# Kernel tuning notes

Measured on AMD Instinct MI355X. Metric: run time of the kernel, lower is better.

## Reference

```python
import jax, jax.numpy as jnp
import numpy as np
from jax import lax

B, N, D, H, E, K, FF = 4, 1024, 1024, 16, 12, 2, 4
HD = D // H
EPS_LN = 1e-5


def setup_inputs() -> dict:
    key = jax.random.key(0)
    ks = jax.random.split(key, 10)
    s = 0.02
    return {
        "x": jax.random.normal(ks[0], (B, N, D), jnp.float32),
        "Wr": jax.random.normal(ks[1], (E, D), jnp.float32) * s,          # router [E, D] (no bias)
        "Wq": jax.random.normal(ks[2], (E, D, D), jnp.float32) * s,       # per-expert [out, in]
        "Wk": jax.random.normal(ks[3], (E, D, D), jnp.float32) * s,
        "Wv": jax.random.normal(ks[4], (E, D, D), jnp.float32) * s,
        "Wo": jax.random.normal(ks[5], (E, D, D), jnp.float32) * s,
        "W1": jax.random.normal(ks[6], (FF * D, D), jnp.float32) * s,
        "b1": jnp.zeros((FF * D,), jnp.float32),
        "W2": jax.random.normal(ks[7], (D, FF * D), jnp.float32) * s,
        "b2": jnp.zeros((D,), jnp.float32),
        "g1": jnp.ones((D,), jnp.float32),
        "be1": jnp.zeros((D,), jnp.float32),
        "g2": jnp.ones((D,), jnp.float32),
        "be2": jnp.zeros((D,), jnp.float32),
    }


def _ln(x, g, b):
    m = jnp.mean(x, axis=-1, keepdims=True)
    v = jnp.mean(jnp.square(x - m), axis=-1, keepdims=True)
    return (x - m) * lax.rsqrt(v + EPS_LN) * g + b


def _moe_mix(inp, W, combine):
    """sum_e combine[:, e] * (inp @ W[e].T) via scan over the E experts.
    inp: [T, Din], W: [E, Dout, Din], combine: [T, E] -> [T, Dout]"""
    def body(acc, ec):
        We, ce = ec
        return acc + ce[:, None] * (inp @ We.T), None
    acc0 = jnp.zeros((inp.shape[0], W.shape[1]), inp.dtype)
    acc, _ = lax.scan(body, acc0, (W, jnp.swapaxes(combine, 0, 1)))
    return acc


def _moe_attention(x, Wr, Wq, Wk, Wv, Wo):
    x_flat = x.reshape(-1, D)                     # [T, D]
    T = x_flat.shape[0]
    logits = x_flat @ Wr.T                        # [T, E]
    probs = jax.nn.softmax(logits, axis=-1)
    topv, topi = lax.top_k(probs, K)              # [T, K]
    topv = topv / (jnp.sum(topv, axis=-1, keepdims=True) + 1e-6)
    # dense combine weights [T, E] (zero for unselected experts)
    combine = jnp.zeros((T, E), x.dtype).at[jnp.arange(T)[:, None], topi].add(topv)

    q = _moe_mix(x_flat, Wq, combine)
    k = _moe_mix(x_flat, Wk, combine)
    v = _moe_mix(x_flat, Wv, combine)

    # [B, H, N, HD]
    q = q.reshape(B, N, H, HD).transpose(0, 2, 1, 3)
    k = k.reshape(B, N, H, HD).transpose(0, 2, 1, 3)
    v = v.reshape(B, N, H, HD).transpose(0, 2, 1, 3)
    scores = jnp.einsum("bhqd,bhkd->bhqk", q, k) / jnp.sqrt(jnp.asarray(HD, x.dtype))
    attn = jax.nn.softmax(scores, axis=-1)
    out = jnp.einsum("bhqk,bhkd->bhqd", attn, v)
    out_flat = out.transpose(0, 2, 1, 3).reshape(T, D)

    o = _moe_mix(out_flat, Wo, combine)           # expert output projection

    # load-balance loss (no grad in original: computed under torch.no_grad)
    counts = jnp.zeros((E,), x.dtype).at[topi.ravel()].add(1.0)
    p = probs.sum(axis=0)
    lb = jax.lax.stop_gradient((counts / (counts.sum() + 1e-6) * p).sum() * E)
    return o.reshape(B, N, D), lb


def reference(x, Wr, Wq, Wk, Wv, Wo, W1, b1, W2, b2, g1, be1, g2, be2):
    # pre-norm transformer block: x + MoEAttn(LN(x)); + FFN(LN(.))
    attn_out, lb = _moe_attention(_ln(x, g1, be1), Wr, Wq, Wk, Wv, Wo)
    h = x + attn_out
    hn = _ln(h, g2, be2)
    ff = (jax.nn.gelu(hn @ W1.T + b1)) @ W2.T + b2   # dropout=0 (eval)
    y = h + ff
    return y, lb
```

## Files before the change

kernel.cpp:

```cpp
#include <hip/hip_runtime.h>

#define B_ 4
#define N_ 1024
#define D_ 1024
#define H_ 16
#define HD_ 64
#define E_ 12
#define T_ 4096
#define FF_ 4096

static constexpr size_t SZ_ = (size_t)T_ * D_;

typedef __attribute__((ext_vector_type(8))) short bhalf8;
typedef __attribute__((ext_vector_type(4))) float f32x4;

#define GLDS(gp, lp)                                                         \
  __builtin_amdgcn_global_load_lds(                                          \
      (const __attribute__((address_space(1))) void*)(gp),                   \
      (__attribute__((address_space(3))) void*)(lp), 16, 0, 0)

__device__ __forceinline__ float wave_sum64(float v) {
#pragma unroll
  for (int o = 32; o > 0; o >>= 1) v += __shfl_down(v, o);
  return v;
}

__device__ __forceinline__ unsigned short f2bf(float f) {
  unsigned u = __float_as_uint(f);
  u += 0x7FFFu + ((u >> 16) & 1u);
  return (unsigned short)(u >> 16);
}
__device__ __forceinline__ float b2f(unsigned short s) {
  return __uint_as_float(((unsigned)s) << 16);
}
__device__ __forceinline__ unsigned addpair_bf(unsigned x, unsigned y) {
  float lo = b2f((unsigned short)(x & 0xffff)) + b2f((unsigned short)(y & 0xffff));
  float hi = b2f((unsigned short)(x >> 16)) + b2f((unsigned short)(y >> 16));
  return (unsigned)f2bf(lo) | ((unsigned)f2bf(hi) << 16);
}

__device__ __forceinline__ float gelu_f(float x) {
  float u = 0.7978845608028654f * (x + 0.044715f * x * x * x);
  u = fminf(fmaxf(u, -15.f), 15.f);
  float e = __expf(2.f * u);
  float th = (e - 1.f) / (e + 1.f);
  return 0.5f * x * (1.f + th);
}

__device__ __forceinline__ int slot_of(int row, int q) {
  return row * 4 + (q ^ ((row >> 1) & 3));
}

__global__ __launch_bounds__(256) void ln_kernel(const float* __restrict__ x,
    const float* __restrict__ g, const float* __restrict__ b,
    float* __restrict__ out, unsigned short* __restrict__ outb) {
  const int t = blockIdx.x, tid = threadIdx.x;
  const size_t base = (size_t)t * D_;
  const float4 v = ((const float4*)(x + base))[tid];
  float s = v.x + v.y + v.z + v.w;
  float s2 = v.x * v.x + v.y * v.y + v.z * v.z + v.w * v.w;
  s = wave_sum64(s);
  s2 = wave_sum64(s2);
  __shared__ float ls[4], ls2[4];
  const int w = tid >> 6;
  if ((tid & 63) == 0) { ls[w] = s; ls2[w] = s2; }
  __syncthreads();
  const float mean = (ls[0] + ls[1] + ls[2] + ls[3]) * (1.0f / D_);
  const float var = (ls2[0] + ls2[1] + ls2[2] + ls2[3]) * (1.0f / D_) - mean * mean;
  const float inv = rsqrtf(var + 1e-5f);
  const float4 gg = ((const float4*)g)[tid];
  const float4 bb = ((const float4*)b)[tid];
  float4 o4;
  o4.x = (v.x - mean) * inv * gg.x + bb.x;
  o4.y = (v.y - mean) * inv * gg.y + bb.y;
  o4.z = (v.z - mean) * inv * gg.z + bb.z;
  o4.w = (v.w - mean) * inv * gg.w + bb.w;
  ((float4*)(out + base))[tid] = o4;
  ushort4 u4;
  u4.x = f2bf(o4.x); u4.y = f2bf(o4.y); u4.z = f2bf(o4.z); u4.w = f2bf(o4.w);
  ((ushort4*)(outb + base))[tid] = u4;
}

__global__ __launch_bounds__(256) void hln2_kernel(const float* __restrict__ x,
    const unsigned short* __restrict__ oa, const unsigned short* __restrict__ ob,
    const float* __restrict__ g, const float* __restrict__ be,
    float* __restrict__ hout, unsigned short* __restrict__ hnb) {
  const int t = blockIdx.x, tid = threadIdx.x;
  const size_t base = (size_t)t * D_;
  const float4 xv = ((const float4*)(x + base))[tid];
  const ushort4 av = ((const ushort4*)(oa + base))[tid];
  const ushort4 bv = ((const ushort4*)(ob + base))[tid];
  float4 hv;
  hv.x = xv.x + b2f(av.x) + b2f(bv.x);
  hv.y = xv.y + b2f(av.y) + b2f(bv.y);
  hv.z = xv.z + b2f(av.z) + b2f(bv.z);
  hv.w = xv.w + b2f(av.w) + b2f(bv.w);
  ((float4*)(hout + base))[tid] = hv;
  float s = hv.x + hv.y + hv.z + hv.w;
  float s2 = hv.x * hv.x + hv.y * hv.y + hv.z * hv.z + hv.w * hv.w;
  s = wave_sum64(s);
  s2 = wave_sum64(s2);
  __shared__ float ls[4], ls2[4];
  const int w = tid >> 6;
  if ((tid & 63) == 0) { ls[w] = s; ls2[w] = s2; }
  __syncthreads();
  const float mean = (ls[0] + ls[1] + ls[2] + ls[3]) * (1.0f / D_);
  const float var = (ls2[0] + ls2[1] + ls2[2] + ls2[3]) * (1.0f / D_) - mean * mean;
  const float inv = rsqrtf(var + 1e-5f);
  const float4 gg = ((const float4*)g)[tid];
  const float4 bb = ((const float4*)be)[tid];
  ushort4 o4;
  o4.x = f2bf((hv.x - mean) * inv * gg.x + bb.x);
  o4.y = f2bf((hv.y - mean) * inv * gg.y + bb.y);
  o4.z = f2bf((hv.z - mean) * inv * gg.z + bb.z);
  o4.w = f2bf((hv.w - mean) * inv * gg.w + bb.w);
  ((ushort4*)(hnb + base))[tid] = o4;
}

__global__ __launch_bounds__(256) void router_logits(const float* __restrict__ xn,
    const float* __restrict__ Wr, float* __restrict__ probs,
    int* __restrict__ topi, float2* __restrict__ topw) {
  const int t = blockIdx.x, tid = threadIdx.x;
  const float4 xv = ((const float4*)(xn + (size_t)t * D_))[tid];
  float acc[E_];
#pragma unroll
  for (int e = 0; e < E_; ++e) {
    const float4 wv = ((const float4*)(Wr + (size_t)e * D_))[tid];
    acc[e] = xv.x * wv.x + xv.y * wv.y + xv.z * wv.z + xv.w * wv.w;
  }
#pragma unroll
  for (int e = 0; e < E_; ++e) acc[e] = wave_sum64(acc[e]);
  __shared__ float red[4][E_];
  const int w = tid >> 6;
  if ((tid & 63) == 0) {
#pragma unroll
    for (int e = 0; e < E_; ++e) red[w][e] = acc[e];
  }
  __syncthreads();
  if (tid == 0) {
    float lg[E_];
    float mx = -1e30f;
#pragma unroll
    for (int e = 0; e < E_; ++e) {
      lg[e] = red[0][e] + red[1][e] + red[2][e] + red[3][e];
      mx = fmaxf(mx, lg[e]);
    }
    float p[E_];
    float sum = 0.f;
#pragma unroll
    for (int e = 0; e < E_; ++e) { p[e] = __expf(lg[e] - mx); sum += p[e]; }
    const float invs = 1.f / sum;
#pragma unroll
    for (int e = 0; e < E_; ++e) {
      p[e] *= invs;
      probs[t * E_ + e] = p[e];
    }
    int i0 = 0;
#pragma unroll
    for (int e = 1; e < E_; ++e) if (p[e] > p[i0]) i0 = e;
    int i1 = (i0 == 0) ? 1 : 0;
#pragma unroll
    for (int e = 0; e < E_; ++e) if (e != i0 && p[e] > p[i1]) i1 = e;
    const float rs = 1.f / (p[i0] + p[i1] + 1e-6f);
    topi[t] = i0 | (i1 << 8);
    topw[t] = make_float2(p[i0] * rs, p[i1] * rs);
  }
}

__global__ __launch_bounds__(256) void psum_kernel(const float* __restrict__ probs,
                                                   float* __restrict__ psum) {
  const int tid = threadIdx.x;
  float local[E_] = {};
  for (int t = tid; t < T_; t += 256) {
#pragma unroll
    for (int e = 0; e < E_; ++e) local[e] += probs[t * E_ + e];
  }
#pragma unroll
  for (int e = 0; e < E_; ++e) local[e] = wave_sum64(local[e]);
  __shared__ float red[4][E_];
  const int w = tid >> 6;
  if ((tid & 63) == 0) {
#pragma unroll
    for (int e = 0; e < E_; ++e) red[w][e] = local[e];
  }
  __syncthreads();
  if (tid < E_)
    psum[tid] = red[0][tid] + red[1][tid] + red[2][tid] + red[3][tid];
}

__global__ __launch_bounds__(256) void build_lists(const int* __restrict__ topi,
    const float2* __restrict__ topw, int* __restrict__ ecnt,
    int* __restrict__ etok, float* __restrict__ ewt) {
  const int e = blockIdx.x;
  const int tid = threadIdx.x;
  const int wid = tid >> 6, lane = tid & 63;
  __shared__ int wbase[4];
  __shared__ int base;
  if (tid == 0) base = 0;
  __syncthreads();
  for (int c = 0; c < T_; c += 256) {
    const int t = c + tid;
    const int pk = topi[t];
    const int i0 = pk & 0xFF, i1 = (pk >> 8) & 0xFF;
    const float2 w2 = topw[t];
    const int sel = (i0 == e) ? 0 : ((i1 == e) ? 1 : -1);
    const unsigned long long mask = __ballot(sel >= 0);
    const int prefix = __popcll(mask & ((1ULL << lane) - 1ULL));
    if (lane == 0) wbase[wid] = __popcll(mask);
    __syncthreads();
    if (tid == 0) {
      int s = base;
#pragma unroll
      for (int ww = 0; ww < 4; ++ww) { int cc = wbase[ww]; wbase[ww] = s; s += cc; }
      base = s;
    }
    __syncthreads();
    if (sel >= 0) {
      const int pos = wbase[wid] + prefix;
      etok[e * T_ + pos] = t | (sel << 16);
      ewt[e * T_ + pos] = sel ? w2.y : w2.x;
    }
    __syncthreads();
  }
  if (tid == 0) ecnt[e] = base;
}

__global__ __launch_bounds__(256) void cvtw_kernel(const float* __restrict__ src,
    unsigned short* __restrict__ dst) {
  const size_t i = (size_t)blockIdx.x * 256 + threadIdx.x;
  const float4 v = ((const float4*)src)[i];
  ushort4 o;
  o.x = f2bf(v.x); o.y = f2bf(v.y); o.z = f2bf(v.z); o.w = f2bf(v.w);
  ((ushort4*)dst)[i] = o;
}

__global__ __launch_bounds__(256) void moe_mfma(const unsigned short* __restrict__ Ab,
    const float* __restrict__ Wall, unsigned short* __restrict__ out,
    size_t kkStride, const int* __restrict__ ecnt, const int* __restrict__ etok,
    const float* __restrict__ ewt) {
  const int e = blockIdx.z;
  const int Me = ecnt[e];
  const int m0 = blockIdx.y * 128;
  if (m0 >= Me) return;
  const int n0 = blockIdx.x * 128;
  const float* W = Wall + (size_t)e * D_ * D_;
  __shared__ __align__(16) unsigned short As[128 * 32];
  __shared__ __align__(16) unsigned short Bs[128 * 32];
  __shared__ int stok[128];
  __shared__ float swt[128];
  const int tid = threadIdx.x;
  if (tid < 128) {
    const int s = m0 + tid;
    if (s < Me) { stok[tid] = etok[e * T_ + s]; swt[tid] = ewt[e * T_ + s]; }
    else        { stok[tid] = 0;                swt[tid] = 0.f; }
  }
  __syncthreads();
  const int s0 = tid, s1 = tid + 256;
  const int r0 = s0 >> 2, q0 = (s0 & 3) ^ ((r0 >> 1) & 3);
  const int r1 = s1 >> 2, q1 = (s1 & 3) ^ ((r1 >> 1) & 3);
  const unsigned short* aP0 = Ab + (size_t)(stok[r0] & 0xFFFF) * D_ + q0 * 8;
  const unsigned short* aP1 = Ab + (size_t)(stok[r1] & 0xFFFF) * D_ + q1 * 8;
  const float* bP0 = W + (size_t)(n0 + r0) * D_ + q0 * 8;
  const float* bP1 = W + (size_t)(n0 + r1) * D_ + q1 * 8;
  char* AsC = (char*)As;
  char* BsC = (char*)Bs;
  const int wave = tid >> 6, lane = tid & 63;
  const int wm0 = (wave >> 1) * 64, wn0 = (wave & 1) * 64;
  const int lr = lane & 15, lq = lane >> 4;
  int aoff[4], boff[4];
#pragma unroll
  for (int t = 0; t < 4; ++t) {
    aoff[t] = slot_of(wm0 + t * 16 + lr, lq) * 16;
    boff[t] = slot_of(wn0 + t * 16 + lr, lq) * 16;
  }
  f32x4 acc[4][4];
#pragma unroll
  for (int i = 0; i < 4; ++i)
#pragma unroll
    for (int j = 0; j < 4; ++j) acc[i][j] = (f32x4){0.f, 0.f, 0.f, 0.f};
  for (int kt = 0; kt < D_; kt += 32) {
    __syncthreads();
    GLDS(aP0 + kt, AsC + s0 * 16);
    GLDS(aP1 + kt, AsC + s1 * 16);
    const float4 f0 = *(const float4*)(bP0 + kt);
    const float4 f1 = *(const float4*)(bP0 + kt + 4);
    const float4 f2 = *(const float4*)(bP1 + kt);
    const float4 f3 = *(const float4*)(bP1 + kt + 4);
    bhalf8 w0, w1;
    w0[0] = (short)f2bf(f0.x); w0[1] = (short)f2bf(f0.y);
    w0[2] = (short)f2bf(f0.z); w0[3] = (short)f2bf(f0.w);
    w0[4] = (short)f2bf(f1.x); w0[5] = (short)f2bf(f1.y);
    w0[6] = (short)f2bf(f1.z); w0[7] = (short)f2bf(f1.w);
    w1[0] = (short)f2bf(f2.x); w1[1] = (short)f2bf(f2.y);
    w1[2] = (short)f2bf(f2.z); w1[3] = (short)f2bf(f2.w);
    w1[4] = (short)f2bf(f3.x); w1[5] = (short)f2bf(f3.y);
    w1[6] = (short)f2bf(f3.z); w1[7] = (short)f2bf(f3.w);
    *(bhalf8*)(BsC + s0 * 16) = w0;
    *(bhalf8*)(BsC + s1 * 16) = w1;
    __syncthreads();
    bhalf8 af[4], bfr[4];
#pragma unroll
    for (int t = 0; t < 4; ++t) af[t] = *(const bhalf8*)(AsC + aoff[t]);
#pragma unroll
    for (int t = 0; t < 4; ++t) bfr[t] = *(const bhalf8*)(BsC + boff[t]);
#pragma unroll
    for (int i = 0; i < 4; ++i)
#pragma unroll
      for (int j = 0; j < 4; ++j)
        acc[i][j] = __builtin_amdgcn_mfma_f32_16x16x32_bf16(af[i], bfr[j], acc[i][j], 0, 0, 0);
  }
#pragma unroll
  for (int mt = 0; mt < 4; ++mt)
#pragma unroll
    for (int nt = 0; nt < 4; ++nt) {
      const f32x4 c = acc[mt][nt];
      const int col = n0 + wn0 + nt * 16 + lr;
#pragma unroll
      for (int r = 0; r < 4; ++r) {
        const int row = wm0 + mt * 16 + lq * 4 + r;
        if (m0 + row < Me) {
          const int pk = stok[row];
          out[(size_t)(pk >> 16) * kkStride + (size_t)(pk & 0xFFFF) * D_ + col] =
              f2bf(c[r] * swt[row]);
        }
      }
    }
}

__global__ __launch_bounds__(256) void ffn1_mfma(const unsigned short* __restrict__ Ab,
    const unsigned short* __restrict__ Bb, const float* __restrict__ bias,
    unsigned short* __restrict__ mid) {
  const int m0 = blockIdx.y * 128, n0 = blockIdx.x * 128;
  __shared__ __align__(16) unsigned short As[128 * 32];
  __shared__ __align__(16) unsigned short Bs[128 * 32];
  const int tid = threadIdx.x;
  const int s0 = tid, s1 = tid + 256;
  const int r0 = s0 >> 2, q0 = (s0 & 3) ^ ((r0 >> 1) & 3);
  const int r1 = s1 >> 2, q1 = (s1 & 3) ^ ((r1 >> 1) & 3);
  const unsigned short* aP0 = Ab + (size_t)(m0 + r0) * D_ + q0 * 8;
  const unsigned short* aP1 = Ab + (size_t)(m0 + r1) * D_ + q1 * 8;
  const unsigned short* bP0 = Bb + (size_t)(n0 + r0) * D_ + q0 * 8;
  const unsigned short* bP1 = Bb + (size_t)(n0 + r1) * D_ + q1 * 8;
  char* AsC = (char*)As;
  char* BsC = (char*)Bs;
  const int wave = tid >> 6, lane = tid & 63;
  const int wm0 = (wave >> 1) * 64, wn0 = (wave & 1) * 64;
  const int lr = lane & 15, lq = lane >> 4;
  int aoff[4], boff[4];
#pragma unroll
  for (int t = 0; t < 4; ++t) {
    aoff[t] = slot_of(wm0 + t * 16 + lr, lq) * 16;
    boff[t] = slot_of(wn0 + t * 16 + lr, lq) * 16;
  }
  f32x4 acc[4][4];
#pragma unroll
  for (int i = 0; i < 4; ++i)
#pragma unroll
    for (int j = 0; j < 4; ++j) acc[i][j] = (f32x4){0.f, 0.f, 0.f, 0.f};
  for (int kt = 0; kt < D_; kt += 32) {
    __syncthreads();
    GLDS(aP0 + kt, AsC + s0 * 16);
    GLDS(aP1 + kt, AsC + s1 * 16);
    GLDS(bP0 + kt, BsC + s0 * 16);
    GLDS(bP1 + kt, BsC + s1 * 16);
    __syncthreads();
    bhalf8 af[4], bfr[4];
#pragma unroll
    for (int t = 0; t < 4; ++t) af[t] = *(const bhalf8*)(AsC + aoff[t]);
#pragma unroll
    for (int t = 0; t < 4; ++t) bfr[t] = *(const bhalf8*)(BsC + boff[t]);
#pragma unroll
    for (int i = 0; i < 4; ++i)
#pragma unroll
      for (int j = 0; j < 4; ++j)
        acc[i][j] = __builtin_amdgcn_mfma_f32_16x16x32_bf16(af[i], bfr[j], acc[i][j], 0, 0, 0);
  }
  float bcol[4];
#pragma unroll
  for (int nt = 0; nt < 4; ++nt) bcol[nt] = bias[n0 + wn0 + nt * 16 + lr];
#pragma unroll
  for (int mt = 0; mt < 4; ++mt)
#pragma unroll
    for (int nt = 0; nt < 4; ++nt) {
      const f32x4 c = acc[mt][nt];
      const int col = n0 + wn0 + nt * 16 + lr;
#pragma unroll
      for (int r = 0; r < 4; ++r) {
        const int row = m0 + wm0 + mt * 16 + lq * 4 + r;
        mid[(size_t)row * FF_ + col] = f2bf(gelu_f(c[r] + bcol[nt]));
      }
    }
}

__global__ __launch_bounds__(256) void ffn2_mfma(const unsigned short* __restrict__ Ab,
    const unsigned short* __restrict__ Bb, const float* __restrict__ bias,
    const float* __restrict__ hres, float* __restrict__ y) {
  const int m0 = blockIdx.y * 128, n0 = blockIdx.x * 128;
  __shared__ __align__(16) unsigned short As[128 * 32];
  __shared__ __align__(16) unsigned short Bs[128 * 32];
  const int tid = threadIdx.x;
  const int s0 = tid, s1 = tid + 256;
  const int r0 = s0 >> 2, q0 = (s0 & 3) ^ ((r0 >> 1) & 3);
  const int r1 = s1 >> 2, q1 = (s1 & 3) ^ ((r1 >> 1) & 3);
  const unsigned short* aP0 = Ab + (size_t)(m0 + r0) * FF_ + q0 * 8;
  const unsigned short* aP1 = Ab + (size_t)(m0 + r1) * FF_ + q1 * 8;
  const unsigned short* bP0 = Bb + (size_t)(n0 + r0) * FF_ + q0 * 8;
  const unsigned short* bP1 = Bb + (size_t)(n0 + r1) * FF_ + q1 * 8;
  char* AsC = (char*)As;
  char* BsC = (char*)Bs;
  const int wave = tid >> 6, lane = tid & 63;
  const int wm0 = (wave >> 1) * 64, wn0 = (wave & 1) * 64;
  const int lr = lane & 15, lq = lane >> 4;
  int aoff[4], boff[4];
#pragma unroll
  for (int t = 0; t < 4; ++t) {
    aoff[t] = slot_of(wm0 + t * 16 + lr, lq) * 16;
    boff[t] = slot_of(wn0 + t * 16 + lr, lq) * 16;
  }
  f32x4 acc[4][4];
#pragma unroll
  for (int i = 0; i < 4; ++i)
#pragma unroll
    for (int j = 0; j < 4; ++j) acc[i][j] = (f32x4){0.f, 0.f, 0.f, 0.f};
  for (int kt = 0; kt < FF_; kt += 32) {
    __syncthreads();
    GLDS(aP0 + kt, AsC + s0 * 16);
    GLDS(aP1 + kt, AsC + s1 * 16);
    GLDS(bP0 + kt, BsC + s0 * 16);
    GLDS(bP1 + kt, BsC + s1 * 16);
    __syncthreads();
    bhalf8 af[4], bfr[4];
#pragma unroll
    for (int t = 0; t < 4; ++t) af[t] = *(const bhalf8*)(AsC + aoff[t]);
#pragma unroll
    for (int t = 0; t < 4; ++t) bfr[t] = *(const bhalf8*)(BsC + boff[t]);
#pragma unroll
    for (int i = 0; i < 4; ++i)
#pragma unroll
      for (int j = 0; j < 4; ++j)
        acc[i][j] = __builtin_amdgcn_mfma_f32_16x16x32_bf16(af[i], bfr[j], acc[i][j], 0, 0, 0);
  }
  float bcol[4];
#pragma unroll
  for (int nt = 0; nt < 4; ++nt) bcol[nt] = bias[n0 + wn0 + nt * 16 + lr];
#pragma unroll
  for (int mt = 0; mt < 4; ++mt)
#pragma unroll
    for (int nt = 0; nt < 4; ++nt) {
      const f32x4 c = acc[mt][nt];
      const int col = n0 + wn0 + nt * 16 + lr;
#pragma unroll
      for (int r = 0; r < 4; ++r) {
        const int row = m0 + wm0 + mt * 16 + lq * 4 + r;
        const size_t idx = (size_t)row * D_ + col;
        y[idx] = c[r] + bcol[nt] + hres[idx];
      }
    }
}

__global__ __launch_bounds__(256) void add2b_kernel(unsigned short* __restrict__ a,
    const unsigned short* __restrict__ b) {
  const size_t i = (size_t)blockIdx.x * 256 + threadIdx.x;
  uint4 av = ((uint4*)a)[i];
  const uint4 bv = ((const uint4*)b)[i];
  av.x = addpair_bf(av.x, bv.x);
  av.y = addpair_bf(av.y, bv.y);
  av.z = addpair_bf(av.z, bv.z);
  av.w = addpair_bf(av.w, bv.w);
  ((uint4*)a)[i] = av;
}

__global__ __launch_bounds__(256) void attn_kernel(const unsigned short* __restrict__ q,
    const unsigned short* __restrict__ k, const unsigned short* __restrict__ v,
    unsigned short* __restrict__ out) {
  const int bh = blockIdx.x;
  const int b = bh >> 4, h = bh & 15;
  const int q0 = blockIdx.y * 64;
  const int tid = threadIdx.x;
  const int wave = tid >> 6, lane = tid & 63;
  const int lc = lane & 15, lg = lane >> 4;

  __shared__ __align__(16) unsigned short Ks[64 * 64];
  __shared__ __align__(16) unsigned short Vt[64 * 64];
  __shared__ __align__(16) unsigned short Pl[4][16 * 64];
  char* const KsC = (char*)Ks;
  char* const VtC = (char*)Vt;
  char* const PlC = (char*)&Pl[wave][0];

  bhalf8 qf0, qf1;
  {
    const unsigned short* qp =
        q + ((size_t)(b * N_ + q0 + wave * 16 + lc)) * D_ + h * HD_ + lg * 8;
    qf0 = *(const bhalf8*)qp;
    qf1 = *(const bhalf8*)(qp + 32);
  }

  int off[4][2];
#pragma unroll
  for (int t = 0; t < 4; ++t)
#pragma unroll
    for (int ch = 0; ch < 2; ++ch)
      off[t][ch] = (t * 16 + lc) * 128 + (((ch * 4 + lg) ^ (lc & 7)) << 4);

  const int krow = tid >> 2, ks0 = tid & 3;
  const unsigned short* const kgp =
      k + ((size_t)(b * N_ + krow)) * D_ + h * HD_ + ks0 * 8;
  const int kwo0 = krow * 128 + ((ks0 ^ (krow & 7)) << 4);
  const int kwo1 = krow * 128 + (((ks0 ^ 4) ^ (krow & 7)) << 4);
  const int vkv = (tid & 31) * 2, vd0 = (tid >> 5) * 8;
  const unsigned short* const vgp =
      v + ((size_t)(b * N_ + vkv)) * D_ + h * HD_ + vd0;
  int vwo[8];
#pragma unroll
  for (int c = 0; c < 8; ++c) {
    const int d = vd0 + c;
    vwo[c] = d * 128 + ((((vkv >> 3) ^ (d & 7)) << 4)) + (vkv & 7) * 2;
  }

  float m_i[4], l_i[4];
  f32x4 o_acc[4];
#pragma unroll
  for (int r = 0; r < 4; ++r) { m_i[r] = -3.0e38f; l_i[r] = 0.f; }
#pragma unroll
  for (int t = 0; t < 4; ++t) o_acc[t] = (f32x4){0.f, 0.f, 0.f, 0.f};

  uint4 ka = *(const uint4*)(kgp);
  uint4 kb = *(const uint4*)(kgp + 32);
  uint4 va = *(const uint4*)(vgp);
  uint4 vb = *(const uint4*)(vgp + D_);

  for (int kt = 0; kt < 16; ++kt) {
    __syncthreads();
    *(uint4*)(KsC + kwo0) = ka;
    *(uint4*)(KsC + kwo1) = kb;
    {
      const unsigned av4[4] = {va.x, va.y, va.z, va.w};
      const unsigned bv4[4] = {vb.x, vb.y, vb.z, vb.w};
#pragma unroll
      for (int c = 0; c < 4; ++c) {
        const unsigned w0 = (av4[c] & 0xffffu) | (bv4[c] << 16);
        const unsigned w1 = (av4[c] >> 16) | (bv4[c] & 0xffff0000u);
        *(unsigned*)(VtC + vwo[2 * c]) = w0;
        *(unsigned*)(VtC + vwo[2 * c + 1]) = w1;
      }
    }
    __syncthreads();
    if (kt < 15) {
      const size_t go = (size_t)(kt + 1) * 64 * D_;
      ka = *(const uint4*)(kgp + go);
      kb = *(const uint4*)(kgp + go + 32);
      va = *(const uint4*)(vgp + go);
      vb = *(const uint4*)(vgp + go + D_);
    }
    f32x4 s4[4];
#pragma unroll
    for (int t = 0; t < 4; ++t) {
      f32x4 acc = (f32x4){0.f, 0.f, 0.f, 0.f};
      acc = __builtin_amdgcn_mfma_f32_16x16x32_bf16(
          qf0, *(const bhalf8*)(KsC + off[t][0]), acc, 0, 0, 0);
      acc = __builtin_amdgcn_mfma_f32_16x16x32_bf16(
          qf1, *(const bhalf8*)(KsC + off[t][1]), acc, 0, 0, 0);
      s4[t] = acc;
    }
    float alpha[4];
#pragma unroll
    for (int r = 0; r < 4; ++r) {
      const float e0 = s4[0][r] * 0.125f, e1 = s4[1][r] * 0.125f;
      const float e2 = s4[2][r] * 0.125f, e3 = s4[3][r] * 0.125f;
      float mt = fmaxf(fmaxf(e0, e1), fmaxf(e2, e3));
#pragma unroll
      for (int o = 8; o > 0; o >>= 1) mt = fmaxf(mt, __shfl_xor(mt, o));
      const float mn = fmaxf(m_i[r], mt);
      alpha[r] = __expf(m_i[r] - mn);
      m_i[r] = mn;
      const float p0 = __expf(e0 - mn), p1 = __expf(e1 - mn);
      const float p2 = __expf(e2 - mn), p3 = __expf(e3 - mn);
      float rs = p0 + p1 + p2 + p3;
#pragma unroll
      for (int o = 8; o > 0; o >>= 1) rs += __shfl_xor(rs, o);
      l_i[r] = l_i[r] * alpha[r] + rs;
      const int qrow = 4 * lg + r;
      const int rb = qrow * 128 + (lc & 7) * 2;
      const int sw = qrow & 7;
      *(unsigned short*)(PlC + rb + (((0 + (lc >> 3)) ^ sw) << 4)) = f2bf(p0);
      *(unsigned short*)(PlC + rb + (((2 + (lc >> 3)) ^ sw) << 4)) = f2bf(p1);
      *(unsigned short*)(PlC + rb + (((4 + (lc >> 3)) ^ sw) << 4)) = f2bf(p2);
      *(unsigned short*)(PlC + rb + (((6 + (lc >> 3)) ^ sw) << 4)) = f2bf(p3);
    }
#pragma unroll
    for (int t = 0; t < 4; ++t) {
      f32x4 o = o_acc[t];
      o[0] *= alpha[0]; o[1] *= alpha[1]; o[2] *= alpha[2]; o[3] *= alpha[3];
      o_acc[t] = o;
    }
    const bhalf8 pf0 = *(const bhalf8*)(PlC + off[0][0]);
    const bhalf8 pf1 = *(const bhalf8*)(PlC + off[0][1]);
#pragma unroll
    for (int t = 0; t < 4; ++t) {
      o_acc[t] = __builtin_amdgcn_mfma_f32_16x16x32_bf16(
          pf0, *(const bhalf8*)(VtC + off[t][0]), o_acc[t], 0, 0, 0);
      o_acc[t] = __builtin_amdgcn_mfma_f32_16x16x32_bf16(
          pf1, *(const bhalf8*)(VtC + off[t][1]), o_acc[t], 0, 0, 0);
    }
  }
  const size_t obase = ((size_t)(b * N_ + q0 + wave * 16)) * D_ + h * HD_;
#pragma unroll
  for (int r = 0; r < 4; ++r) {
    const float inv = 1.f / l_i[r];
    const size_t rbase = obase + (size_t)(4 * lg + r) * D_;
#pragma unroll
    for (int t = 0; t < 4; ++t)
      out[rbase + t * 16 + lc] = f2bf(o_acc[t][r] * inv);
  }
}

__global__ void lb_kernel(const int* __restrict__ ecnt,
                          const float* __restrict__ psum, float* __restrict__ out) {
  if (threadIdx.x == 0 && blockIdx.x == 0) {
    float tot = 0.f;
    for (int e = 0; e < E_; ++e) tot += (float)ecnt[e];
    float s = 0.f;
    for (int e = 0; e < E_; ++e) s += (float)ecnt[e] / (tot + 1e-6f) * psum[e];
    out[0] = s * (float)E_;
  }
}

extern "C" void kernel_launch(void* const* d_in, const int* in_sizes, int n_in,
                              void* d_out, int out_size, void* d_ws, size_t ws_size,
                              hipStream_t stream) {
  (void)in_sizes; (void)n_in; (void)out_size; (void)ws_size;
  const float* x  = (const float*)d_in[0];
  const float* Wr = (const float*)d_in[1];
  const float* Wq = (const float*)d_in[2];
  const float* Wk = (const float*)d_in[3];
  const float* Wv = (const float*)d_in[4];
  const float* Wo = (const float*)d_in[5];
  const float* W1 = (const float*)d_in[6];
  const float* b1 = (const float*)d_in[7];
  const float* W2 = (const float*)d_in[8];
  const float* b2 = (const float*)d_in[9];
  const float* g1 = (const float*)d_in[10];
  const float* be1 = (const float*)d_in[11];
  const float* g2 = (const float*)d_in[12];
  const float* be2 = (const float*)d_in[13];
  float* y = (float*)d_out;

  char* p = (char*)d_ws;
  float* xn = (float*)p;                 p += SZ_ * 4;
  unsigned short* xnb = (unsigned short*)p;  p += SZ_ * 2;
  unsigned short* q2b = (unsigned short*)p;  p += 2 * SZ_ * 2;
  unsigned short* k2b = (unsigned short*)p;  p += 2 * SZ_ * 2;
  unsigned short* v2b = (unsigned short*)p;  p += 2 * SZ_ * 2;
  unsigned short* attb = (unsigned short*)p; p += SZ_ * 2;
  unsigned short* W1b = (unsigned short*)p;  p += (size_t)FF_ * D_ * 2;
  unsigned short* W2b = (unsigned short*)p;  p += (size_t)FF_ * D_ * 2;
  float* psum = (float*)p;               p += E_ * 4;
  int* ecnt = (int*)p;                   p += E_ * 4;
  int* etok = (int*)p;                   p += (size_t)E_ * T_ * 4;
  float* ewt = (float*)p;                p += (size_t)E_ * T_ * 4;
  float* probs = (float*)p;              p += (size_t)T_ * E_ * 4;
  int* topi = (int*)p;                   p += T_ * 4;
  float2* topw = (float2*)p;
  unsigned short* o2b  = q2b;
  float* hbuf          = (float*)k2b;
  unsigned short* hnb  = v2b;
  unsigned short* midb = (unsigned short*)d_ws;

  ln_kernel<<<T_, 256, 0, stream>>>(x, g1, be1, xn, xnb);
  cvtw_kernel<<<(FF_ * D_) / 1024, 256, 0, stream>>>(W1, W1b);
  cvtw_kernel<<<(FF_ * D_) / 1024, 256, 0, stream>>>(W2, W2b);
  router_logits<<<T_, 256, 0, stream>>>(xn, Wr, probs, topi, topw);
  psum_kernel<<<1, 256, 0, stream>>>(probs, psum);
  build_lists<<<E_, 256, 0, stream>>>(topi, topw, ecnt, etok, ewt);
  dim3 gmoe(D_ / 128, T_ / 128, E_);
  moe_mfma<<<gmoe, 256, 0, stream>>>(xnb, Wq, q2b, SZ_, ecnt, etok, ewt);
  moe_mfma<<<gmoe, 256, 0, stream>>>(xnb, Wk, k2b, SZ_, ecnt, etok, ewt);
  moe_mfma<<<gmoe, 256, 0, stream>>>(xnb, Wv, v2b, SZ_, ecnt, etok, ewt);
  add2b_kernel<<<SZ_ / 2048, 256, 0, stream>>>(q2b, q2b + SZ_);
  add2b_kernel<<<SZ_ / 2048, 256, 0, stream>>>(k2b, k2b + SZ_);
  add2b_kernel<<<SZ_ / 2048, 256, 0, stream>>>(v2b, v2b + SZ_);
  attn_kernel<<<dim3(B_ * H_, N_ / 64), 256, 0, stream>>>(q2b, k2b, v2b, attb);
  moe_mfma<<<gmoe, 256, 0, stream>>>(attb, Wo, o2b, SZ_, ecnt, etok, ewt);
  hln2_kernel<<<T_, 256, 0, stream>>>(x, o2b, o2b + SZ_, g2, be2, hbuf, hnb);
  ffn1_mfma<<<dim3(FF_ / 128, T_ / 128), 256, 0, stream>>>(hnb, W1b, b1, midb);
  ffn2_mfma<<<dim3(D_ / 128, T_ / 128), 256, 0, stream>>>(midb, W2b, b2, hbuf, y);
  lb_kernel<<<1, 64, 0, stream>>>(ecnt, psum, y + SZ_);
}
```

Baseline: 734.5 us.

## Pre-convert expert weights to bf16, fuse LN into router, split-K FFN2

Each expert weight stack (Wq/Wk/Wv/Wo) is now converted to bf16 by its own pass into a shared buffer, so moe_mfma can load B tiles directly into LDS instead of converting fp32 inside the inner loop. The router now recomputes LayerNorm itself, which drops the fp32 normalized-activation buffer. The residual plus b2 is written to y early in hln2. FFN2 is split along K into two partial-sum kernels joined by an add3 pass, doubling the grid. The cost is four extra full weight-conversion passes and extra partial-buffer traffic.

Result: faster. 680.8 us (-7.3%).

```diff
diff --git a/kernel.cpp b/kernel.cpp
--- a/kernel.cpp
+++ b/kernel.cpp
@@ -53,7 +53,7 @@
 
 __global__ __launch_bounds__(256) void ln_kernel(const float* __restrict__ x,
     const float* __restrict__ g, const float* __restrict__ b,
-    float* __restrict__ out, unsigned short* __restrict__ outb) {
+    unsigned short* __restrict__ outb) {
   const int t = blockIdx.x, tid = threadIdx.x;
   const size_t base = (size_t)t * D_;
   const float4 v = ((const float4*)(x + base))[tid];
@@ -70,21 +70,19 @@
   const float inv = rsqrtf(var + 1e-5f);
   const float4 gg = ((const float4*)g)[tid];
   const float4 bb = ((const float4*)b)[tid];
-  float4 o4;
-  o4.x = (v.x - mean) * inv * gg.x + bb.x;
-  o4.y = (v.y - mean) * inv * gg.y + bb.y;
-  o4.z = (v.z - mean) * inv * gg.z + bb.z;
-  o4.w = (v.w - mean) * inv * gg.w + bb.w;
-  ((float4*)(out + base))[tid] = o4;
   ushort4 u4;
-  u4.x = f2bf(o4.x); u4.y = f2bf(o4.y); u4.z = f2bf(o4.z); u4.w = f2bf(o4.w);
+  u4.x = f2bf((v.x - mean) * inv * gg.x + bb.x);
+  u4.y = f2bf((v.y - mean) * inv * gg.y + bb.y);
+  u4.z = f2bf((v.z - mean) * inv * gg.z + bb.z);
+  u4.w = f2bf((v.w - mean) * inv * gg.w + bb.w);
   ((ushort4*)(outb + base))[tid] = u4;
 }
 
 __global__ __launch_bounds__(256) void hln2_kernel(const float* __restrict__ x,
     const unsigned short* __restrict__ oa, const unsigned short* __restrict__ ob,
     const float* __restrict__ g, const float* __restrict__ be,
-    float* __restrict__ hout, unsigned short* __restrict__ hnb) {
+    const float* __restrict__ b2, float* __restrict__ y,
+    unsigned short* __restrict__ hnb) {
   const int t = blockIdx.x, tid = threadIdx.x;
   const size_t base = (size_t)t * D_;
   const float4 xv = ((const float4*)(x + base))[tid];
@@ -95,7 +93,11 @@
   hv.y = xv.y + b2f(av.y) + b2f(bv.y);
   hv.z = xv.z + b2f(av.z) + b2f(bv.z);
   hv.w = xv.w + b2f(av.w) + b2f(bv.w);
-  ((float4*)(hout + base))[tid] = hv;
+  const float4 b2v = ((const float4*)b2)[tid];
+  float4 yv;
+  yv.x = hv.x + b2v.x; yv.y = hv.y + b2v.y;
+  yv.z = hv.z + b2v.z; yv.w = hv.w + b2v.w;
+  ((float4*)(y + base))[tid] = yv;
   float s = hv.x + hv.y + hv.z + hv.w;
   float s2 = hv.x * hv.x + hv.y * hv.y + hv.z * hv.z + hv.w * hv.w;
   s = wave_sum64(s);
@@ -117,21 +119,39 @@
   ((ushort4*)(hnb + base))[tid] = o4;
 }
 
-__global__ __launch_bounds__(256) void router_logits(const float* __restrict__ xn,
+__global__ __launch_bounds__(256) void router_ln(const float* __restrict__ x,
+    const float* __restrict__ g, const float* __restrict__ b,
     const float* __restrict__ Wr, float* __restrict__ probs,
     int* __restrict__ topi, float2* __restrict__ topw) {
   const int t = blockIdx.x, tid = threadIdx.x;
-  const float4 xv = ((const float4*)(xn + (size_t)t * D_))[tid];
+  const float4 xv = ((const float4*)(x + (size_t)t * D_))[tid];
+  float s = xv.x + xv.y + xv.z + xv.w;
+  float s2 = xv.x * xv.x + xv.y * xv.y + xv.z * xv.z + xv.w * xv.w;
+  s = wave_sum64(s);
+  s2 = wave_sum64(s2);
+  __shared__ float ls[4], ls2[4];
+  const int w = tid >> 6;
+  if ((tid & 63) == 0) { ls[w] = s; ls2[w] = s2; }
+  __syncthreads();
+  const float mean = (ls[0] + ls[1] + ls[2] + ls[3]) * (1.0f / D_);
+  const float var = (ls2[0] + ls2[1] + ls2[2] + ls2[3]) * (1.0f / D_) - mean * mean;
+  const float inv = rsqrtf(var + 1e-5f);
+  const float4 gg = ((const float4*)g)[tid];
+  const float4 bb = ((const float4*)b)[tid];
+  float4 xn4;
+  xn4.x = (xv.x - mean) * inv * gg.x + bb.x;
+  xn4.y = (xv.y - mean) * inv * gg.y + bb.y;
+  xn4.z = (xv.z - mean) * inv * gg.z + bb.z;
+  xn4.w = (xv.w - mean) * inv * gg.w + bb.w;
   float acc[E_];
 #pragma unroll
   for (int e = 0; e < E_; ++e) {
     const float4 wv = ((const float4*)(Wr + (size_t)e * D_))[tid];
-    acc[e] = xv.x * wv.x + xv.y * wv.y + xv.z * wv.z + xv.w * wv.w;
+    acc[e] = xn4.x * wv.x + xn4.y * wv.y + xn4.z * wv.z + xn4.w * wv.w;
   }
 #pragma unroll
   for (int e = 0; e < E_; ++e) acc[e] = wave_sum64(acc[e]);
   __shared__ float red[4][E_];
-  const int w = tid >> 6;
   if ((tid & 63) == 0) {
 #pragma unroll
     for (int e = 0; e < E_; ++e) red[w][e] = acc[e];
@@ -235,7 +255,7 @@
 }
 
 __global__ __launch_bounds__(256) void moe_mfma(const unsigned short* __restrict__ Ab,
-    const float* __restrict__ Wall, unsigned short* __restrict__ out,
+    const unsigned short* __restrict__ Wb, unsigned short* __restrict__ out,
     size_t kkStride, const int* __restrict__ ecnt, const int* __restrict__ etok,
     const float* __restrict__ ewt) {
   const int e = blockIdx.z;
@@ -243,7 +263,7 @@
   const int m0 = blockIdx.y * 128;
   if (m0 >= Me) return;
   const int n0 = blockIdx.x * 128;
-  const float* W = Wall + (size_t)e * D_ * D_;
+  const unsigned short* W = Wb + (size_t)e * D_ * D_;
   __shared__ __align__(16) unsigned short As[128 * 32];
   __shared__ __align__(16) unsigned short Bs[128 * 32];
   __shared__ int stok[128];
@@ -260,8 +280,8 @@
   const int r1 = s1 >> 2, q1 = (s1 & 3) ^ ((r1 >> 1) & 3);
   const unsigned short* aP0 = Ab + (size_t)(stok[r0] & 0xFFFF) * D_ + q0 * 8;
   const unsigned short* aP1 = Ab + (size_t)(stok[r1] & 0xFFFF) * D_ + q1 * 8;
-  const float* bP0 = W + (size_t)(n0 + r0) * D_ + q0 * 8;
-  const float* bP1 = W + (size_t)(n0 + r1) * D_ + q1 * 8;
+  const unsigned short* bP0 = W + (size_t)(n0 + r0) * D_ + q0 * 8;
+  const unsigned short* bP1 = W + (size_t)(n0 + r1) * D_ + q1 * 8;
   char* AsC = (char*)As;
   char* BsC = (char*)Bs;
   const int wave = tid >> 6, lane = tid & 63;
@@ -282,21 +302,8 @@
     __syncthreads();
     GLDS(aP0 + kt, AsC + s0 * 16);
     GLDS(aP1 + kt, AsC + s1 * 16);
-    const float4 f0 = *(const float4*)(bP0 + kt);
-    const float4 f1 = *(const float4*)(bP0 + kt + 4);
-    const float4 f2 = *(const float4*)(bP1 + kt);
-    const float4 f3 = *(const float4*)(bP1 + kt + 4);
-    bhalf8 w0, w1;
-    w0[0] = (short)f2bf(f0.x); w0[1] = (short)f2bf(f0.y);
-    w0[2] = (short)f2bf(f0.z); w0[3] = (short)f2bf(f0.w);
-    w0[4] = (short)f2bf(f1.x); w0[5] = (short)f2bf(f1.y);
-    w0[6] = (short)f2bf(f1.z); w0[7] = (short)f2bf(f1.w);
-    w1[0] = (short)f2bf(f2.x); w1[1] = (short)f2bf(f2.y);
-    w1[2] = (short)f2bf(f2.z); w1[3] = (short)f2bf(f2.w);
-    w1[4] = (short)f2bf(f3.x); w1[5] = (short)f2bf(f3.y);
-    w1[6] = (short)f2bf(f3.z); w1[7] = (short)f2bf(f3.w);
-    *(bhalf8*)(BsC + s0 * 16) = w0;
-    *(bhalf8*)(BsC + s1 * 16) = w1;
+    GLDS(bP0 + kt, BsC + s0 * 16);
+    GLDS(bP1 + kt, BsC + s1 * 16);
     __syncthreads();
     bhalf8 af[4], bfr[4];
 #pragma unroll
@@ -392,20 +399,22 @@
     }
 }
 
-__global__ __launch_bounds__(256) void ffn2_mfma(const unsigned short* __restrict__ Ab,
-    const unsigned short* __restrict__ Bb, const float* __restrict__ bias,
-    const float* __restrict__ hres, float* __restrict__ y) {
+__global__ __launch_bounds__(256) void ffn2_split(const unsigned short* __restrict__ Ab,
+    const unsigned short* __restrict__ Bb, float* __restrict__ part0,
+    float* __restrict__ part1) {
   const int m0 = blockIdx.y * 128, n0 = blockIdx.x * 128;
+  const int k0 = blockIdx.z * (FF_ / 2);
+  float* const part = blockIdx.z ? part1 : part0;
   __shared__ __align__(16) unsigned short As[128 * 32];
   __shared__ __align__(16) unsigned short Bs[128 * 32];
   const int tid = threadIdx.x;
   const int s0 = tid, s1 = tid + 256;
   const int r0 = s0 >> 2, q0 = (s0 & 3) ^ ((r0 >> 1) & 3);
   const int r1 = s1 >> 2, q1 = (s1 & 3) ^ ((r1 >> 1) & 3);
-  const unsigned short* aP0 = Ab + (size_t)(m0 + r0) * FF_ + q0 * 8;
-  const unsigned short* aP1 = Ab + (size_t)(m0 + r1) * FF_ + q1 * 8;
-  const unsigned short* bP0 = Bb + (size_t)(n0 + r0) * FF_ + q0 * 8;
-  const unsigned short* bP1 = Bb + (size_t)(n0 + r1) * FF_ + q1 * 8;
+  const unsigned short* aP0 = Ab + (size_t)(m0 + r0) * FF_ + q0 * 8 + k0;
+  const unsigned short* aP1 = Ab + (size_t)(m0 + r1) * FF_ + q1 * 8 + k0;
+  const unsigned short* bP0 = Bb + (size_t)(n0 + r0) * FF_ + q0 * 8 + k0;
+  const unsigned short* bP1 = Bb + (size_t)(n0 + r1) * FF_ + q1 * 8 + k0;
   char* AsC = (char*)As;
   char* BsC = (char*)Bs;
   const int wave = tid >> 6, lane = tid & 63;
@@ -422,7 +431,7 @@
   for (int i = 0; i < 4; ++i)
 #pragma unroll
     for (int j = 0; j < 4; ++j) acc[i][j] = (f32x4){0.f, 0.f, 0.f, 0.f};
-  for (int kt = 0; kt < FF_; kt += 32) {
+  for (int kt = 0; kt < FF_ / 2; kt += 32) {
     __syncthreads();
     GLDS(aP0 + kt, AsC + s0 * 16);
     GLDS(aP1 + kt, AsC + s1 * 16);
@@ -440,9 +449,6 @@
       for (int j = 0; j < 4; ++j)
         acc[i][j] = __builtin_amdgcn_mfma_f32_16x16x32_bf16(af[i], bfr[j], acc[i][j], 0, 0, 0);
   }
-  float bcol[4];
-#pragma unroll
-  for (int nt = 0; nt < 4; ++nt) bcol[nt] = bias[n0 + wn0 + nt * 16 + lr];
 #pragma unroll
   for (int mt = 0; mt < 4; ++mt)
 #pragma unroll
@@ -452,10 +458,23 @@
 #pragma unroll
       for (int r = 0; r < 4; ++r) {
         const int row = m0 + wm0 + mt * 16 + lq * 4 + r;
-        const size_t idx = (size_t)row * D_ + col;
-        y[idx] = c[r] + bcol[nt] + hres[idx];
+        part[(size_t)row * D_ + col] = c[r];
       }
     }
+}
+
+__global__ __launch_bounds__(256) void add3_kernel(float* __restrict__ y,
+    const float* __restrict__ p0, const float* __restrict__ p1) {
+  const size_t i = (size_t)blockIdx.x * 256 + threadIdx.x;
+  const float4 a = ((const float4*)y)[i];
+  const float4 u = ((const float4*)p0)[i];
+  const float4 v = ((const float4*)p1)[i];
+  float4 o;
+  o.x = a.x + u.x + v.x;
+  o.y = a.y + u.y + v.y;
+  o.z = a.z + u.z + v.z;
+  o.w = a.w + u.w + v.w;
+  ((float4*)y)[i] = o;
 }
 
 __global__ __launch_bounds__(256) void add2b_kernel(unsigned short* __restrict__ a,
@@ -646,12 +665,11 @@
   float* y = (float*)d_out;
 
   char* p = (char*)d_ws;
-  float* xn = (float*)p;                 p += SZ_ * 4;
+  unsigned short* Rb = (unsigned short*)p;   p += (size_t)E_ * D_ * D_ * 2;
   unsigned short* xnb = (unsigned short*)p;  p += SZ_ * 2;
   unsigned short* q2b = (unsigned short*)p;  p += 2 * SZ_ * 2;
   unsigned short* k2b = (unsigned short*)p;  p += 2 * SZ_ * 2;
   unsigned short* v2b = (unsigned short*)p;  p += 2 * SZ_ * 2;
-  unsigned short* attb = (unsigned short*)p; p += SZ_ * 2;
   unsigned short* W1b = (unsigned short*)p;  p += (size_t)FF_ * D_ * 2;
   unsigned short* W2b = (unsigned short*)p;  p += (size_t)FF_ * D_ * 2;
   float* psum = (float*)p;               p += E_ * 4;
@@ -661,28 +679,36 @@
   float* probs = (float*)p;              p += (size_t)T_ * E_ * 4;
   int* topi = (int*)p;                   p += T_ * 4;
   float2* topw = (float2*)p;
+  unsigned short* attb = v2b + SZ_;
   unsigned short* o2b  = q2b;
-  float* hbuf          = (float*)k2b;
   unsigned short* hnb  = v2b;
+  float* part0         = (float*)k2b;
+  float* part1         = (float*)v2b;
   unsigned short* midb = (unsigned short*)d_ws;
 
-  ln_kernel<<<T_, 256, 0, stream>>>(x, g1, be1, xn, xnb);
+  ln_kernel<<<T_, 256, 0, stream>>>(x, g1, be1, xnb);
   cvtw_kernel<<<(FF_ * D_) / 1024, 256, 0, stream>>>(W1, W1b);
   cvtw_kernel<<<(FF_ * D_) / 1024, 256, 0, stream>>>(W2, W2b);
-  router_logits<<<T_, 256, 0, stream>>>(xn, Wr, probs, topi, topw);
+  router_ln<<<T_, 256, 0, stream>>>(x, g1, be1, Wr, probs, topi, topw);
   psum_kernel<<<1, 256, 0, stream>>>(probs, psum);
   build_lists<<<E_, 256, 0, stream>>>(topi, topw, ecnt, etok, ewt);
   dim3 gmoe(D_ / 128, T_ / 128, E_);
-  moe_mfma<<<gmoe, 256, 0, stream>>>(xnb, Wq, q2b, SZ_, ecnt, etok, ewt);
-  moe_mfma<<<gmoe, 256, 0, stream>>>(xnb, Wk, k2b, SZ_, ecnt, etok, ewt);
-  moe_mfma<<<gmoe, 256, 0, stream>>>(xnb, Wv, v2b, SZ_, ecnt, etok, ewt);
+  const int gw = (E_ * D_ * D_) / 1024;
+  cvtw_kernel<<<gw, 256, 0, stream>>>(Wq, Rb);
+  moe_mfma<<<gmoe, 256, 0, stream>>>(xnb, Rb, q2b, SZ_, ecnt, etok, ewt);
+  cvtw_kernel<<<gw, 256, 0, stream>>>(Wk, Rb);
+  moe_mfma<<<gmoe, 256, 0, stream>>>(xnb, Rb, k2b, SZ_, ecnt, etok, ewt);
+  cvtw_kernel<<<gw, 256, 0, stream>>>(Wv, Rb);
+  moe_mfma<<<gmoe, 256, 0, stream>>>(xnb, Rb, v2b, SZ_, ecnt, etok, ewt);
+  cvtw_kernel<<<gw, 256, 0, stream>>>(Wo, Rb);
   add2b_kernel<<<SZ_ / 2048, 256, 0, stream>>>(q2b, q2b + SZ_);
   add2b_kernel<<<SZ_ / 2048, 256, 0, stream>>>(k2b, k2b + SZ_);
   add2b_kernel<<<SZ_ / 2048, 256, 0, stream>>>(v2b, v2b + SZ_);
   attn_kernel<<<dim3(B_ * H_, N_ / 64), 256, 0, stream>>>(q2b, k2b, v2b, attb);
-  moe_mfma<<<gmoe, 256, 0, stream>>>(attb, Wo, o2b, SZ_, ecnt, etok, ewt);
-  hln2_kernel<<<T_, 256, 0, stream>>>(x, o2b, o2b + SZ_, g2, be2, hbuf, hnb);
+  moe_mfma<<<gmoe, 256, 0, stream>>>(attb, Rb, o2b, SZ_, ecnt, etok, ewt);
+  hln2_kernel<<<T_, 256, 0, stream>>>(x, o2b, o2b + SZ_, g2, be2, b2, y, hnb);
   ffn1_mfma<<<dim3(FF_ / 128, T_ / 128), 256, 0, stream>>>(hnb, W1b, b1, midb);
-  ffn2_mfma<<<dim3(D_ / 128, T_ / 128), 256, 0, stream>>>(midb, W2b, b2, hbuf, y);
+  ffn2_split<<<dim3(D_ / 128, T_ / 128, 2), 256, 0, stream>>>(midb, W2b, part0, part1);
+  add3_kernel<<<SZ_ / 1024, 256, 0, stream>>>(y, part0, part1);
   lb_kernel<<<1, 64, 0, stream>>>(ecnt, psum, y + SZ_);
 }
```
